# Kernel optimization log

Hardware: AMD Instinct MI355X
Metric: run time of the kernel (lower is better)

Reference implementation:

```python
import math
import jax, jax.numpy as jnp
import numpy as np

# ---- model dims ----
D = 4096          # hidden_size
N = 32            # num_attention_heads (== num_key_value_heads)
Q_LORA = 1536
KV_LORA = 512
QK_NOPE = 128
QK_ROPE = 64
QK_HEAD = QK_NOPE + QK_ROPE   # 192
V_HEAD = 128
EPS = 1e-6
T = 2048

# ---- yarn rope constants ----
ROPE_THETA = 10000.0
FACTOR = 40.0
ORIG_MAX = 4096
BETA_FAST = 32.0
BETA_SLOW = 1.0
MSCALE = 1.0
MSCALE_ALL_DIM = 1.0


def _yarn_get_mscale(scale, mscale):
    if scale <= 1.0:
        return 1.0
    return 0.1 * mscale * math.log(scale) + 1.0

# softmax scale: qk_head_dim^-0.5 * yarn_mscale^2 (rope_mscale_all_dim = 1.0)
YARN_MSCALE = _yarn_get_mscale(FACTOR, MSCALE_ALL_DIM)
SM_SCALE = QK_HEAD ** (-0.5) * YARN_MSCALE ** 2


def _yarn_cos_sin(positions):
    """DeepSeek yarn scaled rotary embeddings. positions: int [T]."""
    half = QK_ROPE // 2
    pow_ = np.arange(0, QK_ROPE, 2, dtype=np.float64) / QK_ROPE
    pos_freqs = ROPE_THETA ** pow_
    inv_extra = 1.0 / pos_freqs
    inv_inter = 1.0 / (FACTOR * pos_freqs)

    def corr_dim(n_rot):
        return (QK_ROPE * math.log(ORIG_MAX / (n_rot * 2 * math.pi))) / (2 * math.log(ROPE_THETA))

    low = max(math.floor(corr_dim(BETA_FAST)), 0)
    high = min(math.ceil(corr_dim(BETA_SLOW)), QK_ROPE - 1)
    ramp = np.clip((np.arange(half, dtype=np.float64) - low) / max(high - low, 1e-3), 0.0, 1.0)
    mask = 1.0 - ramp  # 1 where extrapolation
    inv_freq = inv_inter * (1.0 - mask) + inv_extra * mask
    inv_freq = jnp.asarray(inv_freq, jnp.float32)

    mscale_coef = _yarn_get_mscale(FACTOR, MSCALE) / _yarn_get_mscale(FACTOR, MSCALE_ALL_DIM)
    t = positions.astype(jnp.float32)
    freqs = t[:, None] * inv_freq[None, :]          # [T, half]
    return jnp.cos(freqs) * mscale_coef, jnp.sin(freqs) * mscale_coef


def _apply_rope(x_tnh, cos, sin):
    """Neox-style (split halves) rope. x: [T, N, QK_ROPE]; cos/sin: [T, half]."""
    half = QK_ROPE // 2
    x1, x2 = x_tnh[..., :half], x_tnh[..., half:]
    c, s = cos[:, None, :], sin[:, None, :]
    return jnp.concatenate([x1 * c - x2 * s, x1 * s + x2 * c], axis=-1)


def _rms_norm(x, scale, eps=EPS):
    var = jnp.mean(jnp.square(x), axis=-1, keepdims=True)
    return x * jax.lax.rsqrt(var + eps) * scale


def setup_inputs() -> dict:
    key = jax.random.key(0)
    ks = jax.random.split(key, 8)
    std = 0.02
    return {
        "x": jax.random.normal(ks[0], (T, D), jnp.float32),
        "positions": jnp.arange(T, dtype=jnp.int32),
        "w_q_down": jax.random.normal(ks[1], (D, Q_LORA), jnp.float32) * std,
        "q_norm_scale": jnp.ones((Q_LORA,), jnp.float32),
        "w_q_up": jax.random.normal(ks[2], (Q_LORA, N, QK_HEAD), jnp.float32) * std,
        "w_kv_down": jax.random.normal(ks[3], (D, KV_LORA + QK_ROPE), jnp.float32) * std,
        "kv_norm_scale": jnp.ones((KV_LORA,), jnp.float32),
        "w_kv_up": jax.random.normal(ks[4], (KV_LORA, N, QK_NOPE + V_HEAD), jnp.float32) * std,
        "w_o": jax.random.normal(ks[5], (N, V_HEAD, D), jnp.float32) * std,
    }


def reference(x, positions, w_q_down, q_norm_scale, w_q_up, w_kv_down,
              kv_norm_scale, w_kv_up, w_o):
    cos, sin = _yarn_cos_sin(positions)

    # ---- q projection (low rank) ----
    q_ta = _rms_norm(jnp.einsum('td,da->ta', x, w_q_down), q_norm_scale)
    q_tnh = jnp.einsum('ta,anh->tnh', q_ta, w_q_up)            # [T,N,192]
    q_rope = _apply_rope(q_tnh[..., QK_NOPE:], cos, sin)
    q_tnh = jnp.concatenate([q_tnh[..., :QK_NOPE], q_rope], axis=-1)

    # ---- kv projection (compressed latent) ----
    kv_sa = jnp.einsum('sd,da->sa', x, w_kv_down)              # [T, KV_LORA+64]
    k_rope = _apply_rope(kv_sa[:, None, KV_LORA:], cos, sin)   # [T,1,64]
    k_rope = jnp.broadcast_to(k_rope, (x.shape[0], N, QK_ROPE))
    kv_lat = _rms_norm(kv_sa[..., :KV_LORA], kv_norm_scale)
    kv_nope = jnp.einsum('sa,anh->snh', kv_lat, w_kv_up)       # [T,N,256]
    k_snh = jnp.concatenate([kv_nope[..., :QK_NOPE], k_rope], axis=-1)
    v_snh = kv_nope[..., QK_NOPE:]

    # ---- causal attention (prefill; padding to 128-multiple is a no-op) ----
    scores = jnp.einsum('tnh,snh->nts', q_tnh, k_snh) * SM_SCALE
    tpos = jnp.arange(x.shape[0])
    causal = tpos[:, None] >= tpos[None, :]
    scores = jnp.where(causal[None, :, :], scores, jnp.finfo(scores.dtype).min)
    probs = jax.nn.softmax(scores, axis=-1)
    out_tnh = jnp.einsum('nts,snh->tnh', probs, v_snh)

    # ---- output projection ----
    return jnp.einsum('tnh,nhd->td', out_tnh, w_o)
```

## Files before the change

### kernel.cpp

```cpp
#include <hip/hip_runtime.h>
#include <math.h>
#include <stdint.h>

#define T_    2048
#define D_    4096
#define NH_   32
#define QL_   1536
#define KVL_  512
#define ROPE_ 64
#define NOPE_ 128
#define HQK_  192
#define HV_   128
#define KVD_  576
#define NCAT_ 2112

typedef __bf16 bf16x8 __attribute__((ext_vector_type(8)));
typedef __bf16 bf16x4 __attribute__((ext_vector_type(4)));
typedef float f32x4 __attribute__((ext_vector_type(4)));

__device__ __forceinline__ void gload_lds16(const __bf16* g, __bf16* l) {
  __builtin_amdgcn_global_load_lds(
      (const __attribute__((address_space(1))) void*)g,
      (__attribute__((address_space(3))) void*)l, 16, 0, 0);
}

template <typename OutT>
__global__ __launch_bounds__(256, 3) void mfma_gemm_kernel(
    const __bf16* __restrict__ A, const __bf16* __restrict__ Bt,
    OutT* __restrict__ C, int M, int Ncols, int K) {
  __shared__ __bf16 As[128 * 64];
  __shared__ __bf16 Bs[128 * 64];
  const int tid = threadIdx.x;
  const int lane = tid & 63;
  const int w = tid >> 6;
  const int wm = w >> 1, wn = w & 1;
  const int lg = lane >> 4, lj = lane & 15;
  const int bm = blockIdx.y * 128;
  const int bn = blockIdx.x * 128;

  const __bf16* ga[4]; const __bf16* gb[4];
  int ldsoff[4];
  #pragma unroll
  for (int i = 0; i < 4; ++i) {
    int task = i * 256 + tid;
    int r = task >> 3, cl = task & 7;
    int cg = cl ^ (r & 7);
    ga[i] = A  + (size_t)(bm + r) * K + cg * 8;
    gb[i] = Bt + (size_t)(bn + r) * K + cg * 8;
    ldsoff[i] = (i * 256 + w * 64) * 8;
  }

  f32x4 acc[4][4];
  #pragma unroll
  for (int mi = 0; mi < 4; ++mi)
    #pragma unroll
    for (int ni = 0; ni < 4; ++ni) acc[mi][ni] = (f32x4){0.f, 0.f, 0.f, 0.f};

  for (int k0 = 0; k0 < K; k0 += 64) {
    __syncthreads();
    #pragma unroll
    for (int i = 0; i < 4; ++i) gload_lds16(ga[i] + k0, &As[ldsoff[i]]);
    #pragma unroll
    for (int i = 0; i < 4; ++i) gload_lds16(gb[i] + k0, &Bs[ldsoff[i]]);
    __syncthreads();
    #pragma unroll
    for (int kh = 0; kh < 2; ++kh) {
      bf16x8 af[4], bfr[4];
      #pragma unroll
      for (int i = 0; i < 4; ++i) {
        int ra = wm * 64 + i * 16 + lj;
        af[i] = *(const bf16x8*)&As[ra * 64 + ((((kh << 2) + lg) ^ (ra & 7)) << 3)];
      }
      #pragma unroll
      for (int i = 0; i < 4; ++i) {
        int rb = wn * 64 + i * 16 + lj;
        bfr[i] = *(const bf16x8*)&Bs[rb * 64 + ((((kh << 2) + lg) ^ (rb & 7)) << 3)];
      }
      #pragma unroll
      for (int mi = 0; mi < 4; ++mi)
        #pragma unroll
        for (int ni = 0; ni < 4; ++ni)
          acc[mi][ni] = __builtin_amdgcn_mfma_f32_16x16x32_bf16(af[mi], bfr[ni], acc[mi][ni], 0, 0, 0);
    }
  }

  #pragma unroll
  for (int mi = 0; mi < 4; ++mi) {
    #pragma unroll
    for (int r = 0; r < 4; ++r) {
      int row = bm + wm * 64 + mi * 16 + lg * 4 + r;
      #pragma unroll
      for (int ni = 0; ni < 4; ++ni) {
        int col = bn + wn * 64 + ni * 16 + lj;
        if (col < Ncols) C[(size_t)row * Ncols + col] = (OutT)acc[mi][ni][r];
      }
    }
  }
}

__global__ __launch_bounds__(256) void transpose_bf16_kernel(
    const float* __restrict__ B, __bf16* __restrict__ Bt, int K, int N) {
  __shared__ float tile[64][65];
  int n0 = blockIdx.x * 64, k0 = blockIdx.y * 64;
  int tid = threadIdx.x;
  int kr = tid >> 4, nc = (tid & 15) * 4;
  #pragma unroll
  for (int i = 0; i < 4; ++i) {
    int k = kr + i * 16;
    float4 v = make_float4(0.f, 0.f, 0.f, 0.f);
    if (n0 + nc < N) v = *(const float4*)(B + (size_t)(k0 + k) * N + n0 + nc);
    tile[k][nc + 0] = v.x; tile[k][nc + 1] = v.y;
    tile[k][nc + 2] = v.z; tile[k][nc + 3] = v.w;
  }
  __syncthreads();
  int nl = tid >> 4, k4 = (tid & 15) * 4;
  #pragma unroll
  for (int i = 0; i < 4; ++i) {
    int nn = nl + i * 16;
    bf16x4 o;
    o[0] = (__bf16)tile[k4 + 0][nn]; o[1] = (__bf16)tile[k4 + 1][nn];
    o[2] = (__bf16)tile[k4 + 2][nn]; o[3] = (__bf16)tile[k4 + 3][nn];
    *(bf16x4*)(Bt + (size_t)(n0 + nn) * K + k0 + k4) = o;
  }
}

__global__ __launch_bounds__(256) void conv_bf16_kernel(
    const float* __restrict__ in, __bf16* __restrict__ out, int n8) {
  int i = blockIdx.x * 256 + threadIdx.x;
  if (i >= n8) return;
  float4 a = *(const float4*)(in + (size_t)i * 8);
  float4 b = *(const float4*)(in + (size_t)i * 8 + 4);
  bf16x8 v;
  v[0] = (__bf16)a.x; v[1] = (__bf16)a.y; v[2] = (__bf16)a.z; v[3] = (__bf16)a.w;
  v[4] = (__bf16)b.x; v[5] = (__bf16)b.y; v[6] = (__bf16)b.z; v[7] = (__bf16)b.w;
  *(bf16x8*)(out + (size_t)i * 8) = v;
}

__global__ __launch_bounds__(256) void rmsnorm_bf16_kernel(
    const float* __restrict__ in, __bf16* __restrict__ out,
    const float* __restrict__ scale, int len, int in_stride) {
  int row = blockIdx.x;
  const float* x = in + (size_t)row * in_stride;
  __bf16* y = out + (size_t)row * len;
  float ss = 0.f;
  for (int i = threadIdx.x; i < len; i += 256) { float v = x[i]; ss += v * v; }
  __shared__ float red[4];
  #pragma unroll
  for (int o = 32; o > 0; o >>= 1) ss += __shfl_down(ss, o, 64);
  int wid = threadIdx.x >> 6, lane = threadIdx.x & 63;
  if (lane == 0) red[wid] = ss;
  __syncthreads();
  if (threadIdx.x == 0) {
    float t = red[0] + red[1] + red[2] + red[3];
    red[0] = 1.0f / sqrtf(t / (float)len + 1e-6f);
  }
  __syncthreads();
  float r = red[0];
  for (int i = threadIdx.x; i < len; i += 256) y[i] = (__bf16)(x[i] * r * scale[i]);
}

struct InvFreq { float f[32]; };
__global__ __launch_bounds__(256) void rope_table_kernel(
    const int* __restrict__ pos, float* __restrict__ cosT, float* __restrict__ sinT,
    InvFreq invf) {
  int idx = blockIdx.x * 256 + threadIdx.x;
  if (idx >= T_ * 32) return;
  int t = idx >> 5, i = idx & 31;
  float fr = (float)pos[t] * invf.f[i];
  cosT[idx] = cosf(fr);
  sinT[idx] = sinf(fr);
}

__global__ __launch_bounds__(256) void rope_q_kernel(
    __bf16* __restrict__ q, const float* __restrict__ cosT, const float* __restrict__ sinT) {
  int idx = blockIdx.x * 256 + threadIdx.x;
  if (idx >= T_ * NH_ * 32) return;
  int i = idx & 31;
  int tn = idx >> 5;
  int t = tn >> 5;
  __bf16* b = q + (size_t)tn * HQK_ + NOPE_;
  float x1 = (float)b[i], x2 = (float)b[i + 32];
  float c = cosT[t * 32 + i], s = sinT[t * 32 + i];
  b[i]      = (__bf16)(x1 * c - x2 * s);
  b[i + 32] = (__bf16)(x1 * s + x2 * c);
}

__global__ __launch_bounds__(256) void rope_k_kernel(
    const float* __restrict__ src, int stride, const float* __restrict__ cosT,
    const float* __restrict__ sinT, __bf16* __restrict__ k_rope) {
  int idx = blockIdx.x * 256 + threadIdx.x;
  if (idx >= T_ * 32) return;
  int t = idx >> 5, i = idx & 31;
  const float* b = src + (size_t)t * stride;
  float x1 = b[i], x2 = b[i + 32];
  float c = cosT[idx], s = sinT[idx];
  k_rope[t * 64 + i]      = (__bf16)(x1 * c - x2 * s);
  k_rope[t * 64 + i + 32] = (__bf16)(x1 * s + x2 * c);
}

__global__ __launch_bounds__(256) void prep_vt_kernel(
    const __bf16* __restrict__ kv_nopeb, __bf16* __restrict__ Vt) {
  __shared__ __bf16 tile[64][136];
  int s0 = blockIdx.x * 64;
  int n = blockIdx.y;
  int tid = threadIdx.x;
  #pragma unroll
  for (int i = 0; i < 4; ++i) {
    int idx = tid + i * 256;
    int s = idx >> 4, c = idx & 15;
    bf16x8 v = *(const bf16x8*)(kv_nopeb + ((size_t)(s0 + s) * NH_ + n) * 256 + NOPE_ + c * 8);
    *(bf16x8*)&tile[s][c * 8] = v;
  }
  __syncthreads();
  #pragma unroll
  for (int i = 0; i < 8; ++i) {
    int idx = tid + i * 256;
    int h = idx >> 4, s4 = (idx & 15) * 4;
    bf16x4 v;
    v[0] = tile[s4 + 0][h]; v[1] = tile[s4 + 1][h];
    v[2] = tile[s4 + 2][h]; v[3] = tile[s4 + 3][h];
    *(bf16x4*)(Vt + ((size_t)n * HV_ + h) * T_ + s0 + s4) = v;
  }
}

__global__ __launch_bounds__(256, 2) void attn_mfma_kernel(
    const __bf16* __restrict__ q_tnh, const __bf16* __restrict__ kv_nopeb,
    const __bf16* __restrict__ k_rope, const __bf16* __restrict__ Vt,
    __bf16* __restrict__ attn_out, float sm_scale2) {
  __shared__ __bf16 KsL[2][24 * 64 * 8];
  __shared__ __bf16 Vs[8 * 128 * 8];
  __shared__ __bf16 Ps[4][32 * 64];
  const int tid = threadIdx.x;
  const int lane = tid & 63;
  const int w = tid >> 6;
  const int id = blockIdx.x;
  const int j = id >> 3;
  const int p = j >> 2;
  const int n = (id & 7) * 4 + (j & 3);
  const int lg = lane >> 4;
  const int lj = lane & 15;
  const int qtf0 = p, qtf1 = 31 - p;

  const __bf16* kptr[6]; size_t kstep[6]; int klds[6];
  #pragma unroll
  for (int i = 0; i < 6; ++i) {
    int task = i * 256 + tid;
    int c = task >> 6, s = task & 63;
    if (c < 16) { kptr[i] = kv_nopeb + ((size_t)s * NH_ + n) * 256 + c * 8; kstep[i] = (size_t)64 * NH_ * 256; }
    else        { kptr[i] = k_rope + (size_t)s * ROPE_ + (c - 16) * 8;      kstep[i] = (size_t)64 * ROPE_; }
    klds[i] = (i * 256 + w * 64) * 8;
  }
  const __bf16* vptr[4]; int vlds[4];
  #pragma unroll
  for (int i = 0; i < 4; ++i) {
    int task = i * 256 + tid;
    int c = task >> 7, h = task & 127;
    vptr[i] = Vt + ((size_t)n * HV_ + h) * T_ + c * 8;
    vlds[i] = (i * 256 + w * 64) * 8;
  }

  #define STAGE_K(bufIdx)                                                      \
    do {                                                                       \
      __bf16* kb_ = &KsL[bufIdx][0];                                           \
      _Pragma("unroll")                                                        \
      for (int i_ = 0; i_ < 6; ++i_) {                                         \
        gload_lds16(kptr[i_], kb_ + klds[i_]);                                 \
        kptr[i_] += kstep[i_];                                                 \
      }                                                                        \
    } while (0)
  #define STAGE_V()                                                            \
    do {                                                                       \
      _Pragma("unroll")                                                        \
      for (int i_ = 0; i_ < 4; ++i_) {                                         \
        gload_lds16(vptr[i_], &Vs[0] + vlds[i_]);                              \
        vptr[i_] += 64;                                                        \
      }                                                                        \
    } while (0)

  STAGE_K(0);

  bf16x8 qf[2][6];
  #pragma unroll
  for (int f = 0; f < 2; ++f) {
    int t = (f ? qtf1 : qtf0) * 64 + w * 16 + lj;
    const __bf16* qp = q_tnh + ((size_t)t * NH_ + n) * HQK_;
    #pragma unroll
    for (int kk = 0; kk < 6; ++kk) {
      bf16x8 raw = *(const bf16x8*)(qp + kk * 32 + lg * 8);
      bf16x8 v;
      #pragma unroll
      for (int i = 0; i < 8; ++i) v[i] = (__bf16)((float)raw[i] * sm_scale2);
      qf[f][kk] = v;
    }
  }

  f32x4 O[2][8];
  float m_r[2][4], l_r[2][4];
  #pragma unroll
  for (int f = 0; f < 2; ++f) {
    #pragma unroll
    for (int nb = 0; nb < 8; ++nb) O[f][nb] = (f32x4){0.f, 0.f, 0.f, 0.f};
    #pragma unroll
    for (int r = 0; r < 4; ++r) { m_r[f][r] = -1e30f; l_r[f][r] = 0.f; }
  }

  __syncthreads();

  const int nst = 32 - p;
  #pragma unroll 1
  for (int st = 0; st < nst; ++st) {
    const int s0 = st * 64;
    const int cur = st & 1;
    if (st + 1 < nst) STAGE_K(cur ^ 1);
    STAGE_V();
    const __bf16* kb = &KsL[cur][0];
    const bool act0 = (st <= qtf0);

    #pragma unroll
    for (int f = 0; f < 2; ++f) {
      if (f == 0 && !act0) continue;
      const int qt = f ? qtf1 : qtf0;
      const int rowbase = qt * 64 + w * 16;
      f32x4 S[4];
      __builtin_amdgcn_s_setprio(1);
      #pragma unroll
      for (int sb = 0; sb < 4; ++sb) {
        f32x4 acc = (f32x4){0.f, 0.f, 0.f, 0.f};
        int srow = sb * 16 + lj;
        #pragma unroll
        for (int kk = 0; kk < 6; ++kk) {
          int c = kk * 4 + lg;
          bf16x8 b = *(const bf16x8*)&kb[(c * 64 + srow) * 8];
          acc = __builtin_amdgcn_mfma_f32_16x16x32_bf16(qf[f][kk], b, acc, 0, 0, 0);
        }
        S[sb] = acc;
      }
      __builtin_amdgcn_s_setprio(0);
      if (st == qt) {
        #pragma unroll
        for (int sb = 0; sb < 4; ++sb)
          #pragma unroll
          for (int r = 0; r < 4; ++r) {
            int row = rowbase + lg * 4 + r;
            int col = s0 + sb * 16 + lj;
            if (col > row) S[sb][r] = -1e30f;
          }
      }
      float mx[4];
      #pragma unroll
      for (int r = 0; r < 4; ++r) {
        float m2 = fmaxf(fmaxf(S[0][r], S[1][r]), fmaxf(S[2][r], S[3][r]));
        m2 = fmaxf(m2, __shfl_xor(m2, 1));
        m2 = fmaxf(m2, __shfl_xor(m2, 2));
        m2 = fmaxf(m2, __shfl_xor(m2, 4));
        m2 = fmaxf(m2, __shfl_xor(m2, 8));
        mx[r] = m2;
      }
      int need = (mx[0] > m_r[f][0]) | (mx[1] > m_r[f][1]) |
                 (mx[2] > m_r[f][2]) | (mx[3] > m_r[f][3]);
      if (__any(need)) {
        #pragma unroll
        for (int r = 0; r < 4; ++r) {
          float mnew = fmaxf(m_r[f][r], mx[r]);
          float corr = __builtin_amdgcn_exp2f(m_r[f][r] - mnew);
          m_r[f][r] = mnew;
          l_r[f][r] *= corr;
          #pragma unroll
          for (int nb = 0; nb < 8; ++nb) O[f][nb][r] = O[f][nb][r] * corr;
        }
      }
      #pragma unroll
      for (int r = 0; r < 4; ++r) {
        float psum = 0.f;
        #pragma unroll
        for (int sb = 0; sb < 4; ++sb) {
          float pp = __builtin_amdgcn_exp2f(S[sb][r] - m_r[f][r]);
          S[sb][r] = pp;
          psum += pp;
        }
        l_r[f][r] += psum;
      }
      #pragma unroll
      for (int sb = 0; sb < 4; ++sb) {
        int sl = sb * 16 + lj;
        int c = sl >> 3;
        #pragma unroll
        for (int r = 0; r < 4; ++r) {
          int rw = lg * 4 + r;
          Ps[w][(f * 16 + rw) * 64 + ((c ^ (rw & 7)) << 3) + (sl & 7)] = (__bf16)S[sb][r];
        }
      }
    }
    __syncthreads();
    __builtin_amdgcn_s_setprio(1);
    #pragma unroll
    for (int f = 0; f < 2; ++f) {
      if (f == 0 && !act0) continue;
      #pragma unroll
      for (int kk = 0; kk < 2; ++kk) {
        int ca = kk * 4 + lg;
        bf16x8 pa = *(const bf16x8*)&Ps[w][(f * 16 + lj) * 64 + ((ca ^ (lj & 7)) << 3)];
        #pragma unroll
        for (int nb = 0; nb < 8; ++nb) {
          int h = nb * 16 + lj;
          bf16x8 bv = *(const bf16x8*)&Vs[(ca * 128 + h) * 8];
          O[f][nb] = __builtin_amdgcn_mfma_f32_16x16x32_bf16(pa, bv, O[f][nb], 0, 0, 0);
        }
      }
    }
    __builtin_amdgcn_s_setprio(0);
    __syncthreads();
  }

  #pragma unroll
  for (int f = 0; f < 2; ++f) {
    const int qt = f ? qtf1 : qtf0;
    #pragma unroll
    for (int r = 0; r < 4; ++r) {
      float lsum = l_r[f][r];
      lsum += __shfl_xor(lsum, 1);
      lsum += __shfl_xor(lsum, 2);
      lsum += __shfl_xor(lsum, 4);
      lsum += __shfl_xor(lsum, 8);
      float inv = 1.0f / lsum;
      int t = qt * 64 + w * 16 + lg * 4 + r;
      __bf16* dst = attn_out + ((size_t)t * NH_ + n) * HV_;
      #pragma unroll
      for (int nb = 0; nb < 8; ++nb) dst[nb * 16 + lj] = (__bf16)(O[f][nb][r] * inv);
    }
  }
  #undef STAGE_K
  #undef STAGE_V
}

static void compute_inv_freq(float* out) {
  const double theta = 10000.0, factor = 40.0;
  const double PI = 3.14159265358979323846;
  const int rot = ROPE_;
  double low_d  = rot * log(4096.0 / (32.0 * 2.0 * PI)) / (2.0 * log(theta));
  double high_d = rot * log(4096.0 / ( 1.0 * 2.0 * PI)) / (2.0 * log(theta));
  double low = floor(low_d);  if (low < 0) low = 0;
  double high = ceil(high_d); if (high > rot - 1) high = rot - 1;
  for (int i = 0; i < 32; ++i) {
    double pf = pow(theta, (2.0 * i) / (double)rot);
    double inv_extra = 1.0 / pf;
    double inv_inter = 1.0 / (factor * pf);
    double ramp = ((double)i - low) / fmax(high - low, 0.001);
    ramp = fmin(fmax(ramp, 0.0), 1.0);
    double mask = 1.0 - ramp;
    out[i] = (float)(inv_inter * (1.0 - mask) + inv_extra * mask);
  }
}

extern "C" void kernel_launch(void* const* d_in, const int* in_sizes, int n_in,
                              void* d_out, int out_size, void* d_ws, size_t ws_size,
                              hipStream_t stream) {
  const float* x            = (const float*)d_in[0];
  const int*   positions    = (const int*)d_in[1];
  const float* w_q_down     = (const float*)d_in[2];
  const float* q_norm_scale = (const float*)d_in[3];
  const float* w_q_up       = (const float*)d_in[4];
  const float* w_kv_down    = (const float*)d_in[5];
  const float* kv_norm_scale= (const float*)d_in[6];
  const float* w_kv_up      = (const float*)d_in[7];
  const float* w_o          = (const float*)d_in[8];
  float* out = (float*)d_out;

  float* ws = (float*)d_ws;
  float*  cosT     = ws;
  float*  sinT     = ws + 65536;
  float*  cat      = ws + 131072;
  __bf16* xb       = (__bf16*)(ws + 4456448);
  __bf16* Bt_cat   = (__bf16*)(ws + 8650752);
  __bf16* Bt_qu    = (__bf16*)(ws + 13107200);
  __bf16* Bt_kvu   = (__bf16*)(ws + 17825792);
  __bf16* q_tab    = (__bf16*)(ws + 19922944);
  __bf16* kv_latb  = (__bf16*)(ws + 21495808);
  __bf16* k_ropeb  = (__bf16*)(ws + 22020096);
  __bf16* q_tnhb   = (__bf16*)(ws + 22085632);
  __bf16* kv_nopeb = (__bf16*)(ws + 28377088);
  __bf16* Vt       = (__bf16*)(ws + 13107200);
  __bf16* attn_ob  = (__bf16*)(ws + 17825792);
  __bf16* Bt_o     = (__bf16*)(ws + 4456448);
  (void)ws_size; (void)n_in; (void)in_sizes; (void)out_size;

  InvFreq invf;
  compute_inv_freq(invf.f);
  double ym = 0.1 * log(40.0) + 1.0;
  float sm_scale2 = (float)((ym * ym / sqrt((double)HQK_)) * 1.44269504088896340736);

  rope_table_kernel<<<(T_ * 32 + 255) / 256, 256, 0, stream>>>(positions, cosT, sinT, invf);
  conv_bf16_kernel<<<T_ * D_ / 8 / 256, 256, 0, stream>>>(x, xb, T_ * D_ / 8);
  transpose_bf16_kernel<<<dim3(QL_ / 64, D_ / 64), 256, 0, stream>>>(w_q_down, Bt_cat, D_, QL_);
  transpose_bf16_kernel<<<dim3(KVD_ / 64, D_ / 64), 256, 0, stream>>>(w_kv_down, Bt_cat + (size_t)QL_ * D_, D_, KVD_);
  transpose_bf16_kernel<<<dim3(NH_ * HQK_ / 64, QL_ / 64), 256, 0, stream>>>(w_q_up, Bt_qu, QL_, NH_ * HQK_);
  transpose_bf16_kernel<<<dim3(NH_ * 256 / 64, KVL_ / 64), 256, 0, stream>>>(w_kv_up, Bt_kvu, KVL_, NH_ * 256);

  mfma_gemm_kernel<float><<<dim3((NCAT_ + 127) / 128, T_ / 128), 256, 0, stream>>>(xb, Bt_cat, cat, T_, NCAT_, D_);

  rmsnorm_bf16_kernel<<<T_, 256, 0, stream>>>(cat, q_tab, q_norm_scale, QL_, NCAT_);
  mfma_gemm_kernel<__bf16><<<dim3(NH_ * HQK_ / 128, T_ / 128), 256, 0, stream>>>(q_tab, Bt_qu, q_tnhb, T_, NH_ * HQK_, QL_);
  rope_q_kernel<<<(T_ * NH_ * 32 + 255) / 256, 256, 0, stream>>>(q_tnhb, cosT, sinT);

  rmsnorm_bf16_kernel<<<T_, 256, 0, stream>>>(cat + QL_, kv_latb, kv_norm_scale, KVL_, NCAT_);
  rope_k_kernel<<<(T_ * 32 + 255) / 256, 256, 0, stream>>>(cat + QL_ + KVL_, NCAT_, cosT, sinT, k_ropeb);
  mfma_gemm_kernel<__bf16><<<dim3(NH_ * 256 / 128, T_ / 128), 256, 0, stream>>>(kv_latb, Bt_kvu, kv_nopeb, T_, NH_ * 256, KVL_);

  prep_vt_kernel<<<dim3(T_ / 64, NH_), 256, 0, stream>>>(kv_nopeb, Vt);
  attn_mfma_kernel<<<512, 256, 0, stream>>>(q_tnhb, kv_nopeb, k_ropeb, Vt, attn_ob, sm_scale2);

  transpose_bf16_kernel<<<dim3(D_ / 64, NH_ * HV_ / 64), 256, 0, stream>>>(w_o, Bt_o, NH_ * HV_, D_);
  mfma_gemm_kernel<float><<<dim3(D_ / 128, T_ / 128), 256, 0, stream>>>(attn_ob, Bt_o, out, T_, D_, NH_ * HV_);
}
```

Measured before the change: 413.9 us.

## Add double-buffered 8-wave 128x256 GEMM kernel for up-projections and output projection

Introduces a new 512-thread GEMM kernel with a 128x256 tile, double-buffered LDS for A and B, split-phase MFMA over two halves of the M tile, and s_setprio around the MFMA bursts. Global loads for the next tile are issued while the current one is computed. The q-up, kv-up and output projection GEMMs switch to this kernel. The larger tile cuts redundant A/B loads and the pipelining hides load latency. In exchange it runs only one block per CU and launches fewer blocks (e.g. 8x16=128 for kv-up), which may underfill the 256 CUs.

```diff
diff --git a/kernel.cpp b/kernel.cpp
--- a/kernel.cpp
+++ b/kernel.cpp
@@ -22,6 +22,151 @@
   __builtin_amdgcn_global_load_lds(
       (const __attribute__((address_space(1))) void*)g,
       (__attribute__((address_space(3))) void*)l, 16, 0, 0);
+}
+
+template <typename OutT>
+__global__ __launch_bounds__(512, 1) void mfma_gemm8_kernel(
+    const __bf16* __restrict__ A, const __bf16* __restrict__ Bt,
+    OutT* __restrict__ C, int M, int Ncols, int K) {
+  __shared__ __bf16 As[2][128 * 64];
+  __shared__ __bf16 Bs[2][256 * 64];
+  const int tid = threadIdx.x;
+  const int lane = tid & 63;
+  const int w = tid >> 6;
+  const int wm = w >> 2, wn = w & 3;
+  const int lg = lane >> 4, lj = lane & 15;
+  const int bm = blockIdx.y * 128;
+  const int bn = blockIdx.x * 256;
+
+  const __bf16* ga[2]; int la_off[2];
+  #pragma unroll
+  for (int i = 0; i < 2; ++i) {
+    int task = i * 512 + tid;
+    int r = task >> 3, cl = task & 7;
+    int cg = cl ^ (r & 7);
+    ga[i] = A + (size_t)(bm + r) * K + cg * 8;
+    la_off[i] = (i * 512 + w * 64) * 8;
+  }
+  const __bf16* gb[4]; int lb_off[4];
+  #pragma unroll
+  for (int i = 0; i < 4; ++i) {
+    int task = i * 512 + tid;
+    int r = task >> 3, cl = task & 7;
+    int cg = cl ^ (r & 7);
+    gb[i] = Bt + (size_t)(bn + r) * K + cg * 8;
+    lb_off[i] = (i * 512 + w * 64) * 8;
+  }
+
+  #define SG_A(buf)                                                            \
+    do {                                                                       \
+      _Pragma("unroll")                                                        \
+      for (int i_ = 0; i_ < 2; ++i_) {                                         \
+        gload_lds16(ga[i_], &As[buf][la_off[i_]]);                             \
+        ga[i_] += 64;                                                          \
+      }                                                                        \
+    } while (0)
+  #define SG_B(buf)                                                            \
+    do {                                                                       \
+      _Pragma("unroll")                                                        \
+      for (int i_ = 0; i_ < 4; ++i_) {                                         \
+        gload_lds16(gb[i_], &Bs[buf][lb_off[i_]]);                             \
+        gb[i_] += 64;                                                          \
+      }                                                                        \
+    } while (0)
+
+  f32x4 acc[4][4];
+  #pragma unroll
+  for (int mi = 0; mi < 4; ++mi)
+    #pragma unroll
+    for (int ni = 0; ni < 4; ++ni) acc[mi][ni] = (f32x4){0.f, 0.f, 0.f, 0.f};
+
+  const int NT = K >> 6;
+
+  SG_A(0);
+  SG_B(0);
+  if (NT > 1) {
+    SG_B(1);
+    asm volatile("s_waitcnt vmcnt(4)" ::: "memory");
+  } else {
+    asm volatile("s_waitcnt vmcnt(0)" ::: "memory");
+  }
+  __builtin_amdgcn_s_barrier();
+
+  #pragma unroll 1
+  for (int t = 0; t < NT; ++t) {
+    const int b = t & 1, o = b ^ 1;
+    bf16x8 bfr[4][2], af[2][2];
+    #pragma unroll
+    for (int ni = 0; ni < 4; ++ni) {
+      int rb = wn * 64 + ni * 16 + lj;
+      #pragma unroll
+      for (int kkk = 0; kkk < 2; ++kkk)
+        bfr[ni][kkk] = *(const bf16x8*)&Bs[b][rb * 64 + (((kkk * 4 + lg) ^ (rb & 7)) << 3)];
+    }
+    #pragma unroll
+    for (int mi = 0; mi < 2; ++mi) {
+      int ra = wm * 64 + mi * 16 + lj;
+      #pragma unroll
+      for (int kkk = 0; kkk < 2; ++kkk)
+        af[mi][kkk] = *(const bf16x8*)&As[b][ra * 64 + (((kkk * 4 + lg) ^ (ra & 7)) << 3)];
+    }
+    if (t + 1 < NT) SG_A(o);
+    __builtin_amdgcn_s_barrier();
+    asm volatile("s_waitcnt lgkmcnt(0)" ::: "memory");
+    __builtin_amdgcn_sched_barrier(0);
+    __builtin_amdgcn_s_setprio(1);
+    #pragma unroll
+    for (int mi = 0; mi < 2; ++mi)
+      #pragma unroll
+      for (int ni = 0; ni < 4; ++ni)
+        #pragma unroll
+        for (int kkk = 0; kkk < 2; ++kkk)
+          acc[mi][ni] = __builtin_amdgcn_mfma_f32_16x16x32_bf16(af[mi][kkk], bfr[ni][kkk], acc[mi][ni], 0, 0, 0);
+    __builtin_amdgcn_s_setprio(0);
+    __builtin_amdgcn_s_barrier();
+    bf16x8 af2[2][2];
+    #pragma unroll
+    for (int mi = 0; mi < 2; ++mi) {
+      int ra = wm * 64 + (mi + 2) * 16 + lj;
+      #pragma unroll
+      for (int kkk = 0; kkk < 2; ++kkk)
+        af2[mi][kkk] = *(const bf16x8*)&As[b][ra * 64 + (((kkk * 4 + lg) ^ (ra & 7)) << 3)];
+    }
+    if (t + 2 < NT) {
+      SG_B(b);
+      asm volatile("s_waitcnt vmcnt(4)" ::: "memory");
+    } else {
+      asm volatile("s_waitcnt vmcnt(0)" ::: "memory");
+    }
+    __builtin_amdgcn_s_barrier();
+    asm volatile("s_waitcnt lgkmcnt(0)" ::: "memory");
+    __builtin_amdgcn_sched_barrier(0);
+    __builtin_amdgcn_s_setprio(1);
+    #pragma unroll
+    for (int mi = 0; mi < 2; ++mi)
+      #pragma unroll
+      for (int ni = 0; ni < 4; ++ni)
+        #pragma unroll
+        for (int kkk = 0; kkk < 2; ++kkk)
+          acc[mi + 2][ni] = __builtin_amdgcn_mfma_f32_16x16x32_bf16(af2[mi][kkk], bfr[ni][kkk], acc[mi + 2][ni], 0, 0, 0);
+    __builtin_amdgcn_s_setprio(0);
+    __builtin_amdgcn_s_barrier();
+  }
+
+  #pragma unroll
+  for (int mi = 0; mi < 4; ++mi) {
+    #pragma unroll
+    for (int r = 0; r < 4; ++r) {
+      int row = bm + wm * 64 + mi * 16 + lg * 4 + r;
+      #pragma unroll
+      for (int ni = 0; ni < 4; ++ni) {
+        int col = bn + wn * 64 + ni * 16 + lj;
+        C[(size_t)row * Ncols + col] = (OutT)acc[mi][ni][r];
+      }
+    }
+  }
+  #undef SG_A
+  #undef SG_B
 }
 
 template <typename OutT>
@@ -499,16 +644,16 @@
   mfma_gemm_kernel<float><<<dim3((NCAT_ + 127) / 128, T_ / 128), 256, 0, stream>>>(xb, Bt_cat, cat, T_, NCAT_, D_);
 
   rmsnorm_bf16_kernel<<<T_, 256, 0, stream>>>(cat, q_tab, q_norm_scale, QL_, NCAT_);
-  mfma_gemm_kernel<__bf16><<<dim3(NH_ * HQK_ / 128, T_ / 128), 256, 0, stream>>>(q_tab, Bt_qu, q_tnhb, T_, NH_ * HQK_, QL_);
+  mfma_gemm8_kernel<__bf16><<<dim3(NH_ * HQK_ / 256, T_ / 128), 512, 0, stream>>>(q_tab, Bt_qu, q_tnhb, T_, NH_ * HQK_, QL_);
   rope_q_kernel<<<(T_ * NH_ * 32 + 255) / 256, 256, 0, stream>>>(q_tnhb, cosT, sinT);
 
   rmsnorm_bf16_kernel<<<T_, 256, 0, stream>>>(cat + QL_, kv_latb, kv_norm_scale, KVL_, NCAT_);
   rope_k_kernel<<<(T_ * 32 + 255) / 256, 256, 0, stream>>>(cat + QL_ + KVL_, NCAT_, cosT, sinT, k_ropeb);
-  mfma_gemm_kernel<__bf16><<<dim3(NH_ * 256 / 128, T_ / 128), 256, 0, stream>>>(kv_latb, Bt_kvu, kv_nopeb, T_, NH_ * 256, KVL_);
+  mfma_gemm8_kernel<__bf16><<<dim3(NH_ * 256 / 256, T_ / 128), 512, 0, stream>>>(kv_latb, Bt_kvu, kv_nopeb, T_, NH_ * 256, KVL_);
 
   prep_vt_kernel<<<dim3(T_ / 64, NH_), 256, 0, stream>>>(kv_nopeb, Vt);
   attn_mfma_kernel<<<512, 256, 0, stream>>>(q_tnhb, kv_nopeb, k_ropeb, Vt, attn_ob, sm_scale2);
 
   transpose_bf16_kernel<<<dim3(D_ / 64, NH_ * HV_ / 64), 256, 0, stream>>>(w_o, Bt_o, NH_ * HV_, D_);
-  mfma_gemm_kernel<float><<<dim3(D_ / 128, T_ / 128), 256, 0, stream>>>(attn_ob, Bt_o, out, T_, D_, NH_ * HV_);
-}
+  mfma_gemm8_kernel<float><<<dim3(D_ / 256, T_ / 128), 512, 0, stream>>>(attn_ob, Bt_o, out, T_, D_, NH_ * HV_);
+}
```

New measurement: 439.7 us. +6.2%, slower.
